# Kernel optimization log

Hardware: AMD Instinct MI355X
Metric: run time of the kernel (lower is better)

Reference implementation:

```python
import jax, jax.numpy as jnp
import numpy as np
from jax import lax

B, L, D = 2, 1024, 1024
INTER = 2816  # _find_multiple(round(4.0*1024*2/3), 256)
K, PAD = 3, 1
S = 32  # sqrt(L)
K2 = K * K


def setup_inputs() -> dict:
    key = jax.random.key(0)
    ks = jax.random.split(key, 7)
    x = jax.random.normal(ks[0], (B, L, D), dtype=jnp.float32)
    w_gate_up = jax.random.normal(ks[1], (2 * INTER, D), dtype=jnp.float32) / np.sqrt(D)
    w_metric = jax.random.normal(ks[2], (7, INTER, 3, 3), dtype=jnp.float32) / np.sqrt(INTER * 9)
    b_metric = jax.random.normal(ks[3], (7,), dtype=jnp.float32) * 0.01
    conv_w = jax.random.normal(ks[4], (INTER, 1, K, K), dtype=jnp.float32) / K
    conv_b = jnp.zeros((INTER,), dtype=jnp.float32)
    w_down = jax.random.normal(ks[5], (D, INTER), dtype=jnp.float32) / np.sqrt(INTER)
    return {"x": x, "w_gate_up": w_gate_up, "w_metric": w_metric,
            "b_metric": b_metric, "conv_w": conv_w, "conv_b": conv_b,
            "w_down": w_down}


def _metric_offsets(x2d, w_metric, b_metric):
    # Finsler-Randers style metric: 2x2 linear map M, drift vector, tanh scale.
    p = lax.conv_general_dilated(x2d, w_metric, (1, 1), 'SAME',
                                 dimension_numbers=('NCHW', 'OIHW', 'NCHW'))
    p = p + b_metric[None, :, None, None]  # [B,7,S,S]
    m00, m01, m10, m11 = p[:, 0], p[:, 1], p[:, 2], p[:, 3]
    dr_y, dr_x = p[:, 4], p[:, 5]
    scale = jnp.tanh(p[:, 6])
    ky = (jnp.arange(K) - PAD).astype(x2d.dtype)
    py = jnp.repeat(ky, K)   # (K2,) kernel-tap dy
    px = jnp.tile(ky, K)     # (K2,) kernel-tap dx
    pyb = py[None, :, None, None]
    pxb = px[None, :, None, None]
    off_y = scale[:, None] * (m00[:, None] * pyb + m01[:, None] * pxb) + dr_y[:, None]
    off_x = scale[:, None] * (m10[:, None] * pyb + m11[:, None] * pxb) + dr_x[:, None]
    return off_y, off_x, py, px  # offsets: [B,K2,S,S]


def _deform_depthwise(x2d, off_y, off_x, py, px, conv_w, conv_b):
    # Sampling positions per output pixel & kernel tap: [B,K2,S,S]
    iy = jnp.arange(S, dtype=x2d.dtype)
    pos_y = iy[None, None, :, None] + py[None, :, None, None] + off_y
    pos_x = iy[None, None, None, :] + px[None, :, None, None] + off_x
    y0 = jnp.floor(pos_y)
    x0 = jnp.floor(pos_x)
    ty = pos_y - y0
    tx = pos_x - x0
    y0i = y0.astype(jnp.int32)
    x0i = x0.astype(jnp.int32)
    flat = x2d.reshape(B, INTER, S * S)

    def corner(yy, xx):
        valid = ((yy >= 0) & (yy < S) & (xx >= 0) & (xx < S)).astype(x2d.dtype)
        idx = (jnp.clip(yy, 0, S - 1) * S + jnp.clip(xx, 0, S - 1)).reshape(B, 1, -1)
        v = jnp.take_along_axis(flat, idx, axis=2).reshape(B, INTER, K2, S, S)
        return v * valid[:, None]

    w00 = ((1 - ty) * (1 - tx))[:, None]
    w01 = ((1 - ty) * tx)[:, None]
    w10 = (ty * (1 - tx))[:, None]
    w11 = (ty * tx)[:, None]
    acc = w00 * corner(y0i, x0i)
    acc = acc + w01 * corner(y0i, x0i + 1)
    acc = acc + w10 * corner(y0i + 1, x0i)
    acc = acc + w11 * corner(y0i + 1, x0i + 1)
    out = jnp.einsum('bckij,ck->bcij', acc, conv_w.reshape(INTER, K2))
    return out + conv_b[None, :, None, None]


def reference(x, w_gate_up, w_metric, b_metric, conv_w, conv_b, w_down):
    gu = jnp.einsum('bld,fd->blf', x, w_gate_up)          # [B,L,2*inter]
    gate, up = jnp.split(gu, 2, axis=-1)
    x_ffn = jax.nn.silu(gate) * up                         # [B,L,inter]
    x2d = x_ffn.transpose(0, 2, 1).reshape(B, INTER, S, S)
    off_y, off_x, py, px = _metric_offsets(x2d, w_metric, b_metric)
    out2d = _deform_depthwise(x2d, off_y, off_x, py, px, conv_w, conv_b)
    grid_out = out2d.reshape(B, INTER, L).transpose(0, 2, 1)
    return jnp.einsum('blf,df->bld', grid_out, w_down)
```

## Files before the change

### kernel.cpp

```cpp
#include <hip/hip_runtime.h>
#include <hip/hip_bf16.h>
#include <cstdint>
#include <cstddef>
#include <type_traits>

#define INTER 2816

typedef __bf16 bf16x8 __attribute__((ext_vector_type(8)));
typedef float f32x4 __attribute__((ext_vector_type(4)));
typedef unsigned short u16x8 __attribute__((ext_vector_type(8)));
using bf16 = __hip_bfloat16;
using u16 = unsigned short;

__device__ __forceinline__ u16 f2bu(float f) {
  bf16 h = __float2bfloat16(f);
  return *reinterpret_cast<u16*>(&h);
}
__device__ __forceinline__ float bu2f(u16 u) {
  bf16 h = *reinterpret_cast<bf16*>(&u);
  return __bfloat162float(h);
}

__device__ __forceinline__ void async16(const u16* g, u16* l) {
  __builtin_amdgcn_global_load_lds(
      (const __attribute__((address_space(1))) unsigned int*)g,
      (__attribute__((address_space(3))) unsigned int*)l, 16, 0, 0);
}

__device__ __forceinline__ void stage8(u16* dst, const float* src) {
  const float4 a = *(const float4*)(src);
  const float4 b = *(const float4*)(src + 4);
  u16 tmp[8] = {f2bu(a.x), f2bu(a.y), f2bu(a.z), f2bu(a.w),
                f2bu(b.x), f2bu(b.y), f2bu(b.z), f2bu(b.w)};
  *(uint4*)dst = *(uint4*)tmp;
}

__global__ __launch_bounds__(256)
void prep_all(const float* __restrict__ x, const float* __restrict__ wgu,
              const float* __restrict__ wd, const float* __restrict__ w_metric,
              const float* __restrict__ conv_w, u16* __restrict__ xbf,
              u16* __restrict__ wgubf, u16* __restrict__ wdbf,
              u16* __restrict__ wm2, float* __restrict__ cwT) {
  constexpr size_t S0 = (size_t)2048 * 1024;
  constexpr size_t S1 = (size_t)5632 * 1024;
  constexpr size_t S2 = (size_t)1024 * 2816;
  constexpr size_t NCONV_THREADS = (S0 + S1 + S2) / 8;
  const size_t t = (size_t)blockIdx.x * 256 + threadIdx.x;
  if (t < NCONV_THREADS) {
    const size_t e0 = t * 8;
    const float* src;
    u16* dst;
    size_t off;
    if (e0 < S0) {
      src = x; dst = xbf; off = e0;
    } else if (e0 < S0 + S1) {
      src = wgu; dst = wgubf; off = e0 - S0;
    } else {
      src = wd; dst = wdbf; off = e0 - S0 - S1;
    }
    stage8(dst + off, src + off);
  } else {
    const unsigned p = (unsigned)(t - NCONV_THREADS);
    const unsigned y = p / 2816u;
    const unsigned c = p - y * 2816u;
    if (y < 128) {
      float v = 0.f;
      if (y < 63) {
        const unsigned o = y / 9, tap = y - o * 9;
        v = w_metric[((size_t)o * INTER + c) * 9 + tap];
      }
      wm2[(size_t)y * INTER + c] = f2bu(v);
    } else {
      const unsigned k = y - 128;
      cwT[(size_t)k * INTER + c] = conv_w[(size_t)c * 9 + k];
    }
  }
}

template <typename OT>
__global__ __launch_bounds__(256, 3)
void gemm_nt(const u16* __restrict__ A, int lda, const u16* __restrict__ Bt,
             int ldb, OT* __restrict__ C, int M, int ldc, int K) {
  __shared__ u16 As[128 * 32];
  __shared__ u16 Bs[128 * 32];
  const size_t koff = (size_t)blockIdx.z * K;
  A += koff;
  Bt += koff;
  C += (size_t)blockIdx.z * M * ldc;
  const int m0 = blockIdx.x * 128;
  const int n0 = blockIdx.y * 128;
  const int tid = threadIdx.x;
  const int lane = tid & 63;
  const int wv = tid >> 6;
  const int wm = wv & 1, wn = wv >> 1;
  const int lr = lane & 15;
  const int lq = lane >> 4;

  f32x4 acc[4][4];
#pragma unroll
  for (int i = 0; i < 4; ++i)
#pragma unroll
    for (int j = 0; j < 4; ++j) acc[i][j] = (f32x4){0.f, 0.f, 0.f, 0.f};

  const int srow = tid >> 2;
  const int scol = (tid & 3) * 8;
  const u16* gA0 = A + (size_t)(m0 + srow) * lda + scol;
  const u16* gA1 = A + (size_t)(m0 + 64 + srow) * lda + scol;
  const u16* gB0 = Bt + (size_t)(n0 + srow) * ldb + scol;
  const u16* gB1 = Bt + (size_t)(n0 + 64 + srow) * ldb + scol;
  u16* lA0 = As + tid * 8;
  u16* lA1 = As + 2048 + tid * 8;
  u16* lB0 = Bs + tid * 8;
  u16* lB1 = Bs + 2048 + tid * 8;

  for (int kb = 0; kb < K; kb += 32) {
    async16(gA0 + kb, lA0);
    async16(gA1 + kb, lA1);
    async16(gB0 + kb, lB0);
    async16(gB1 + kb, lB1);
    __syncthreads();
    bf16x8 af[4], bfr[4];
#pragma unroll
    for (int i = 0; i < 4; ++i)
      af[i] = *(const bf16x8*)(&As[(wm * 64 + i * 16 + lr) * 32 + lq * 8]);
#pragma unroll
    for (int j = 0; j < 4; ++j)
      bfr[j] = *(const bf16x8*)(&Bs[(wn * 64 + j * 16 + lr) * 32 + lq * 8]);
#pragma unroll
    for (int i = 0; i < 4; ++i)
#pragma unroll
      for (int j = 0; j < 4; ++j)
        acc[i][j] = __builtin_amdgcn_mfma_f32_16x16x32_bf16(af[i], bfr[j],
                                                            acc[i][j], 0, 0, 0);
    __syncthreads();
  }

#pragma unroll
  for (int i = 0; i < 4; ++i)
#pragma unroll
    for (int j = 0; j < 4; ++j) {
      const int col = n0 + wn * 64 + j * 16 + lr;
#pragma unroll
      for (int r = 0; r < 4; ++r) {
        const int row = m0 + wm * 64 + i * 16 + lq * 4 + r;
        const float v = acc[i][j][r];
        if constexpr (std::is_same_v<OT, float>) {
          C[(size_t)row * ldc + col] = v;
        } else {
          C[(size_t)row * ldc + col] = f2bu(v);
        }
      }
    }
}

__global__ void reduce4(const float* __restrict__ q2, float* __restrict__ out) {
  const size_t i = ((size_t)blockIdx.x * 256 + threadIdx.x) * 4;
  const size_t S = (size_t)2048 * 1024;
  float4 a = *(const float4*)(q2 + i);
  const float4 b = *(const float4*)(q2 + S + i);
  const float4 c = *(const float4*)(q2 + 2 * S + i);
  const float4 d = *(const float4*)(q2 + 3 * S + i);
  a.x += b.x + c.x + d.x;
  a.y += b.y + c.y + d.y;
  a.z += b.z + c.z + d.z;
  a.w += b.w + c.w + d.w;
  *(float4*)(out + i) = a;
}

__global__ __launch_bounds__(256, 3)
void gateup_gemm(const u16* __restrict__ x, const u16* __restrict__ wgu,
                 u16* __restrict__ xffn) {
  constexpr int K = 1024;
  __shared__ u16 As[128 * 32];
  __shared__ u16 Bgs[64 * 32];
  __shared__ u16 Bus[64 * 32];
  const int m0 = blockIdx.x * 128;
  const int n0 = blockIdx.y * 64;
  const int tid = threadIdx.x;
  const int lane = tid & 63;
  const int wv = tid >> 6;
  const int wm = wv & 1, wn = wv >> 1;
  const int lr = lane & 15;
  const int lq = lane >> 4;

  f32x4 accg[4][2], accu[4][2];
#pragma unroll
  for (int i = 0; i < 4; ++i)
#pragma unroll
    for (int j = 0; j < 2; ++j) {
      accg[i][j] = (f32x4){0.f, 0.f, 0.f, 0.f};
      accu[i][j] = (f32x4){0.f, 0.f, 0.f, 0.f};
    }

  const int srow = tid >> 2;
  const int scol = (tid & 3) * 8;
  const u16* gA0 = x + (size_t)(m0 + srow) * K + scol;
  const u16* gA1 = x + (size_t)(m0 + 64 + srow) * K + scol;
  const u16* gBg = wgu + (size_t)(n0 + srow) * K + scol;
  const u16* gBu = wgu + (size_t)(INTER + n0 + srow) * K + scol;
  u16* lA0 = As + tid * 8;
  u16* lA1 = As + 2048 + tid * 8;
  u16* lBg = Bgs + tid * 8;
  u16* lBu = Bus + tid * 8;

  for (int kb = 0; kb < K; kb += 32) {
    async16(gA0 + kb, lA0);
    async16(gA1 + kb, lA1);
    async16(gBg + kb, lBg);
    async16(gBu + kb, lBu);
    __syncthreads();
    bf16x8 af[4], bg[2], bu[2];
#pragma unroll
    for (int i = 0; i < 4; ++i)
      af[i] = *(const bf16x8*)(&As[(wm * 64 + i * 16 + lr) * 32 + lq * 8]);
#pragma unroll
    for (int j = 0; j < 2; ++j) {
      bg[j] = *(const bf16x8*)(&Bgs[(wn * 32 + j * 16 + lr) * 32 + lq * 8]);
      bu[j] = *(const bf16x8*)(&Bus[(wn * 32 + j * 16 + lr) * 32 + lq * 8]);
    }
#pragma unroll
    for (int i = 0; i < 4; ++i)
#pragma unroll
      for (int j = 0; j < 2; ++j) {
        accg[i][j] = __builtin_amdgcn_mfma_f32_16x16x32_bf16(af[i], bg[j],
                                                             accg[i][j], 0, 0, 0);
        accu[i][j] = __builtin_amdgcn_mfma_f32_16x16x32_bf16(af[i], bu[j],
                                                             accu[i][j], 0, 0, 0);
      }
    __syncthreads();
  }

#pragma unroll
  for (int i = 0; i < 4; ++i)
#pragma unroll
    for (int j = 0; j < 2; ++j) {
      const int col = n0 + wn * 32 + j * 16 + lr;
#pragma unroll
      for (int r = 0; r < 4; ++r) {
        const int row = m0 + wm * 64 + i * 16 + lq * 4 + r;
        const float g = accg[i][j][r];
        const float u = accu[i][j][r];
        const float s = g / (1.f + __expf(-g));
        xffn[(size_t)row * INTER + col] = f2bu(s * u);
      }
    }
}

__global__ __launch_bounds__(64)
void offsets_fused(const float* __restrict__ q,
                   const float* __restrict__ b_metric,
                   int4* __restrict__ samp) {
  __shared__ float lds[130 * 65];
  const int chunk = blockIdx.x;
  const int b = chunk >> 4;
  const int c0 = (chunk & 15) * 64;
  const int t = threadIdx.x;

  for (int v = t; v < 130 * 16; v += 64) {
    const int row = v >> 4;
    const int c4 = (v & 15) * 4;
    int pg = c0 - 33 + row;
    pg = min(max(pg, 0), 1023);
    const float* src = q + ((size_t)b * 1024 + pg) * 128 + c4;
    float4 s = *(const float4*)(src);
#pragma unroll
    for (int ks = 1; ks < 8; ++ks) {
      const float4 vv = *(const float4*)(src + (size_t)ks * 2048 * 128);
      s.x += vv.x; s.y += vv.y; s.z += vv.z; s.w += vv.w;
    }
    float* d = &lds[row * 65 + c4];
    d[0] = s.x; d[1] = s.y; d[2] = s.z; d[3] = s.w;
  }
  __syncthreads();

  const int pix = c0 + t;
  const int i = pix >> 5, j = pix & 31;
  float p[7];
#pragma unroll
  for (int o = 0; o < 7; ++o) p[o] = b_metric[o];
#pragma unroll
  for (int tap = 0; tap < 9; ++tap) {
    const int dy = tap / 3 - 1, dx = tap % 3 - 1;
    const int ii = i + dy, jj = j + dx;
    if ((unsigned)ii < 32u && (unsigned)jj < 32u) {
      const float* r = &lds[(t + 33 + dy * 32 + dx) * 65 + tap];
#pragma unroll
      for (int o = 0; o < 7; ++o) p[o] += r[o * 9];
    }
  }
  const float m00 = p[0], m01 = p[1], m10 = p[2], m11 = p[3];
  const float dry = p[4], drx = p[5];
  const float sc = tanhf(p[6]);
#pragma unroll
  for (int k = 0; k < 9; ++k) {
    const float pyk = (float)(k / 3 - 1), pxk = (float)(k % 3 - 1);
    const float offy = sc * (m00 * pyk + m01 * pxk) + dry;
    const float offx = sc * (m10 * pyk + m11 * pxk) + drx;
    const float posy = (float)i + pyk + offy;
    const float posx = (float)j + pxk + offx;
    const float y0f = floorf(posy), x0f = floorf(posx);
    int4 s;
    s.x = (int)y0f;
    s.y = (int)x0f;
    s.z = __float_as_int(posy - y0f);
    s.w = __float_as_int(posx - x0f);
    samp[((size_t)b * 9 + k) * 1024 + pix] = s;
  }
}

__global__ __launch_bounds__(256)
void deform_kernel(const u16* __restrict__ xffn,
                   const int4* __restrict__ samp,
                   const float* __restrict__ cwT,
                   const float* __restrict__ conv_b,
                   u16* __restrict__ gridout) {
  const unsigned t = blockIdx.x * 256 + threadIdx.x;
  const unsigned pix = t / 352u;
  const unsigned cv = t - pix * 352u;
  const int c0 = cv * 8;
  const int b = pix >> 10, l = pix & 1023;

  float acc[8];
  {
    const float4 b0 = *(const float4*)(&conv_b[c0]);
    const float4 b1 = *(const float4*)(&conv_b[c0 + 4]);
    acc[0] = b0.x; acc[1] = b0.y; acc[2] = b0.z; acc[3] = b0.w;
    acc[4] = b1.x; acc[5] = b1.y; acc[6] = b1.z; acc[7] = b1.w;
  }
  const size_t pixbase = (size_t)b * 1024;
#pragma unroll
  for (int k = 0; k < 9; ++k) {
    const int4 s = samp[((size_t)b * 9 + k) * 1024 + l];
    const int y0 = s.x, x0 = s.y;
    const float ty = __int_as_float(s.z), tx = __int_as_float(s.w);
    const int y1 = y0 + 1, x1 = x0 + 1;
    const float vy0 = ((unsigned)y0 < 32u) ? 1.f : 0.f;
    const float vy1 = ((unsigned)y1 < 32u) ? 1.f : 0.f;
    const float vx0 = ((unsigned)x0 < 32u) ? 1.f : 0.f;
    const float vx1 = ((unsigned)x1 < 32u) ? 1.f : 0.f;
    const float w00 = (1.f - ty) * (1.f - tx) * vy0 * vx0;
    const float w01 = (1.f - ty) * tx * vy0 * vx1;
    const float w10 = ty * (1.f - tx) * vy1 * vx0;
    const float w11 = ty * tx * vy1 * vx1;
    const int cy0 = min(max(y0, 0), 31), cy1 = min(max(y1, 0), 31);
    const int cx0 = min(max(x0, 0), 31), cx1 = min(max(x1, 0), 31);
    const u16x8 v00 = *(const u16x8*)(&xffn[(pixbase + cy0 * 32 + cx0) * INTER + c0]);
    const u16x8 v01 = *(const u16x8*)(&xffn[(pixbase + cy0 * 32 + cx1) * INTER + c0]);
    const u16x8 v10 = *(const u16x8*)(&xffn[(pixbase + cy1 * 32 + cx0) * INTER + c0]);
    const u16x8 v11 = *(const u16x8*)(&xffn[(pixbase + cy1 * 32 + cx1) * INTER + c0]);
    const float4 cwa = *(const float4*)(&cwT[(size_t)k * INTER + c0]);
    const float4 cwb = *(const float4*)(&cwT[(size_t)k * INTER + c0 + 4]);
    const float cw[8] = {cwa.x, cwa.y, cwa.z, cwa.w, cwb.x, cwb.y, cwb.z, cwb.w};
#pragma unroll
    for (int e = 0; e < 8; ++e) {
      const float bl = w00 * bu2f(v00[e]) + w01 * bu2f(v01[e]) +
                       w10 * bu2f(v10[e]) + w11 * bu2f(v11[e]);
      acc[e] += bl * cw[e];
    }
  }
  u16 outv[8];
#pragma unroll
  for (int e = 0; e < 8; ++e) outv[e] = f2bu(acc[e]);
  *(uint4*)(&gridout[(pixbase + l) * INTER + c0]) = *(uint4*)outv;
}

extern "C" void kernel_launch(void* const* d_in, const int* in_sizes, int n_in,
                              void* d_out, int out_size, void* d_ws,
                              size_t ws_size, hipStream_t stream) {
  const float* x         = (const float*)d_in[0];
  const float* w_gate_up = (const float*)d_in[1];
  const float* w_metric  = (const float*)d_in[2];
  const float* b_metric  = (const float*)d_in[3];
  const float* conv_w    = (const float*)d_in[4];
  const float* conv_b    = (const float*)d_in[5];
  const float* w_down    = (const float*)d_in[6];
  float* out = (float*)d_out;

  char* w = (char*)d_ws;
  u16* gridout  = (u16*)(w);
  float* q2     = (float*)(w + (12u << 20));
  u16* xffn     = (u16*)(w + (12u << 20));
  u16* xbf      = (u16*)(w + (24u << 20));
  u16* wgubf    = (u16*)(w + (28u << 20) + (256u << 10));
  float* q_conv = (float*)(w + (28u << 20) + (256u << 10));
  u16* wm2      = (u16*)(w + (40u << 20));
  float* cwT    = (float*)(w + (41u << 20));
  int4* samp    = (int4*)(w + (42u << 20));
  u16* wdbf     = (u16*)(w + (44u << 20));

  prep_all<<<6755, 256, 0, stream>>>(x, w_gate_up, w_down, w_metric, conv_w,
                                     xbf, wgubf, wdbf, wm2, cwT);
  gateup_gemm<<<dim3(16, 44), 256, 0, stream>>>(xbf, wgubf, xffn);
  gemm_nt<float><<<dim3(16, 1, 8), 256, 0, stream>>>(
      xffn, INTER, wm2, INTER, q_conv, 2048, 128, 352);
  offsets_fused<<<32, 64, 0, stream>>>(q_conv, b_metric, samp);
  deform_kernel<<<2816, 256, 0, stream>>>(xffn, samp, cwT, conv_b, gridout);
  gemm_nt<float><<<dim3(16, 8, 4), 256, 0, stream>>>(
      gridout, INTER, wdbf, INTER, q2, 2048, 1024, 704);
  reduce4<<<2048, 256, 0, stream>>>(q2, out);
}
```

Before: 211.1 us.

## Replace split-K partial buffer and reduce kernel with atomics; widen gate-up tile

The down-projection split-K GEMM now adds its partial results straight into the zeroed output with float atomics. This drops the 4-slice fp32 partial buffer and the separate reduce4 kernel, at the cost of a memset and atomic traffic. The gate/up GEMM tile also grows from 64 to 128 columns, doubling the accumulators per wave and lowering occupancy to 2 blocks. The larger tile is meant to raise arithmetic intensity per loaded A tile.

Result: slower. 234.6 us (+11.1%).

```diff
diff --git a/kernel.cpp b/kernel.cpp
--- a/kernel.cpp
+++ b/kernel.cpp
@@ -77,7 +77,7 @@
   }
 }
 
-template <typename OT>
+template <typename OT, bool ATOMIC>
 __global__ __launch_bounds__(256, 3)
 void gemm_nt(const u16* __restrict__ A, int lda, const u16* __restrict__ Bt,
              int ldb, OT* __restrict__ C, int M, int ldc, int K) {
@@ -86,7 +86,7 @@
   const size_t koff = (size_t)blockIdx.z * K;
   A += koff;
   Bt += koff;
-  C += (size_t)blockIdx.z * M * ldc;
+  if constexpr (!ATOMIC) C += (size_t)blockIdx.z * M * ldc;
   const int m0 = blockIdx.x * 128;
   const int n0 = blockIdx.y * 128;
   const int tid = threadIdx.x;
@@ -144,7 +144,9 @@
       for (int r = 0; r < 4; ++r) {
         const int row = m0 + wm * 64 + i * 16 + lq * 4 + r;
         const float v = acc[i][j][r];
-        if constexpr (std::is_same_v<OT, float>) {
+        if constexpr (ATOMIC) {
+          unsafeAtomicAdd((float*)&C[(size_t)row * ldc + col], v);
+        } else if constexpr (std::is_same_v<OT, float>) {
           C[(size_t)row * ldc + col] = v;
         } else {
           C[(size_t)row * ldc + col] = f2bu(v);
@@ -153,29 +155,15 @@
     }
 }
 
-__global__ void reduce4(const float* __restrict__ q2, float* __restrict__ out) {
-  const size_t i = ((size_t)blockIdx.x * 256 + threadIdx.x) * 4;
-  const size_t S = (size_t)2048 * 1024;
-  float4 a = *(const float4*)(q2 + i);
-  const float4 b = *(const float4*)(q2 + S + i);
-  const float4 c = *(const float4*)(q2 + 2 * S + i);
-  const float4 d = *(const float4*)(q2 + 3 * S + i);
-  a.x += b.x + c.x + d.x;
-  a.y += b.y + c.y + d.y;
-  a.z += b.z + c.z + d.z;
-  a.w += b.w + c.w + d.w;
-  *(float4*)(out + i) = a;
-}
-
-__global__ __launch_bounds__(256, 3)
+__global__ __launch_bounds__(256, 2)
 void gateup_gemm(const u16* __restrict__ x, const u16* __restrict__ wgu,
                  u16* __restrict__ xffn) {
   constexpr int K = 1024;
   __shared__ u16 As[128 * 32];
-  __shared__ u16 Bgs[64 * 32];
-  __shared__ u16 Bus[64 * 32];
+  __shared__ u16 Bgs[128 * 32];
+  __shared__ u16 Bus[128 * 32];
   const int m0 = blockIdx.x * 128;
-  const int n0 = blockIdx.y * 64;
+  const int n0 = blockIdx.y * 128;
   const int tid = threadIdx.x;
   const int lane = tid & 63;
   const int wv = tid >> 6;
@@ -183,11 +171,11 @@
   const int lr = lane & 15;
   const int lq = lane >> 4;
 
-  f32x4 accg[4][2], accu[4][2];
+  f32x4 accg[4][4], accu[4][4];
 #pragma unroll
   for (int i = 0; i < 4; ++i)
 #pragma unroll
-    for (int j = 0; j < 2; ++j) {
+    for (int j = 0; j < 4; ++j) {
       accg[i][j] = (f32x4){0.f, 0.f, 0.f, 0.f};
       accu[i][j] = (f32x4){0.f, 0.f, 0.f, 0.f};
     }
@@ -196,32 +184,38 @@
   const int scol = (tid & 3) * 8;
   const u16* gA0 = x + (size_t)(m0 + srow) * K + scol;
   const u16* gA1 = x + (size_t)(m0 + 64 + srow) * K + scol;
-  const u16* gBg = wgu + (size_t)(n0 + srow) * K + scol;
-  const u16* gBu = wgu + (size_t)(INTER + n0 + srow) * K + scol;
+  const u16* gBg0 = wgu + (size_t)(n0 + srow) * K + scol;
+  const u16* gBg1 = wgu + (size_t)(n0 + 64 + srow) * K + scol;
+  const u16* gBu0 = wgu + (size_t)(INTER + n0 + srow) * K + scol;
+  const u16* gBu1 = wgu + (size_t)(INTER + n0 + 64 + srow) * K + scol;
   u16* lA0 = As + tid * 8;
   u16* lA1 = As + 2048 + tid * 8;
-  u16* lBg = Bgs + tid * 8;
-  u16* lBu = Bus + tid * 8;
+  u16* lBg0 = Bgs + tid * 8;
+  u16* lBg1 = Bgs + 2048 + tid * 8;
+  u16* lBu0 = Bus + tid * 8;
+  u16* lBu1 = Bus + 2048 + tid * 8;
 
   for (int kb = 0; kb < K; kb += 32) {
     async16(gA0 + kb, lA0);
     async16(gA1 + kb, lA1);
-    async16(gBg + kb, lBg);
-    async16(gBu + kb, lBu);
+    async16(gBg0 + kb, lBg0);
+    async16(gBg1 + kb, lBg1);
+    async16(gBu0 + kb, lBu0);
+    async16(gBu1 + kb, lBu1);
     __syncthreads();
-    bf16x8 af[4], bg[2], bu[2];
+    bf16x8 af[4], bg[4], bu[4];
 #pragma unroll
     for (int i = 0; i < 4; ++i)
       af[i] = *(const bf16x8*)(&As[(wm * 64 + i * 16 + lr) * 32 + lq * 8]);
 #pragma unroll
-    for (int j = 0; j < 2; ++j) {
-      bg[j] = *(const bf16x8*)(&Bgs[(wn * 32 + j * 16 + lr) * 32 + lq * 8]);
-      bu[j] = *(const bf16x8*)(&Bus[(wn * 32 + j * 16 + lr) * 32 + lq * 8]);
+    for (int j = 0; j < 4; ++j) {
+      bg[j] = *(const bf16x8*)(&Bgs[(wn * 64 + j * 16 + lr) * 32 + lq * 8]);
+      bu[j] = *(const bf16x8*)(&Bus[(wn * 64 + j * 16 + lr) * 32 + lq * 8]);
     }
 #pragma unroll
     for (int i = 0; i < 4; ++i)
 #pragma unroll
-      for (int j = 0; j < 2; ++j) {
+      for (int j = 0; j < 4; ++j) {
         accg[i][j] = __builtin_amdgcn_mfma_f32_16x16x32_bf16(af[i], bg[j],
                                                              accg[i][j], 0, 0, 0);
         accu[i][j] = __builtin_amdgcn_mfma_f32_16x16x32_bf16(af[i], bu[j],
@@ -233,8 +227,8 @@
 #pragma unroll
   for (int i = 0; i < 4; ++i)
 #pragma unroll
-    for (int j = 0; j < 2; ++j) {
-      const int col = n0 + wn * 32 + j * 16 + lr;
+    for (int j = 0; j < 4; ++j) {
+      const int col = n0 + wn * 64 + j * 16 + lr;
 #pragma unroll
       for (int r = 0; r < 4; ++r) {
         const int row = m0 + wm * 64 + i * 16 + lq * 4 + r;
@@ -378,7 +372,6 @@
 
   char* w = (char*)d_ws;
   u16* gridout  = (u16*)(w);
-  float* q2     = (float*)(w + (12u << 20));
   u16* xffn     = (u16*)(w + (12u << 20));
   u16* xbf      = (u16*)(w + (24u << 20));
   u16* wgubf    = (u16*)(w + (28u << 20) + (256u << 10));
@@ -388,14 +381,14 @@
   int4* samp    = (int4*)(w + (42u << 20));
   u16* wdbf     = (u16*)(w + (44u << 20));
 
+  hipMemsetAsync(out, 0, (size_t)2048 * 1024 * sizeof(float), stream);
   prep_all<<<6755, 256, 0, stream>>>(x, w_gate_up, w_down, w_metric, conv_w,
                                      xbf, wgubf, wdbf, wm2, cwT);
-  gateup_gemm<<<dim3(16, 44), 256, 0, stream>>>(xbf, wgubf, xffn);
-  gemm_nt<float><<<dim3(16, 1, 8), 256, 0, stream>>>(
+  gateup_gemm<<<dim3(16, 22), 256, 0, stream>>>(xbf, wgubf, xffn);
+  gemm_nt<float, false><<<dim3(16, 1, 8), 256, 0, stream>>>(
       xffn, INTER, wm2, INTER, q_conv, 2048, 128, 352);
   offsets_fused<<<32, 64, 0, stream>>>(q_conv, b_metric, samp);
   deform_kernel<<<2816, 256, 0, stream>>>(xffn, samp, cwT, conv_b, gridout);
-  gemm_nt<float><<<dim3(16, 8, 4), 256, 0, stream>>>(
-      gridout, INTER, wdbf, INTER, q2, 2048, 1024, 704);
-  reduce4<<<2048, 256, 0, stream>>>(q2, out);
-}
+  gemm_nt<float, true><<<dim3(16, 8, 4), 256, 0, stream>>>(
+      gridout, INTER, wdbf, INTER, out, 2048, 1024, 704);
+}
```

## Double-buffer LDS tiles in both GEMM kernels to overlap loads with MFMA

Applied to the files above, without the earlier changes.

Both bf16 GEMM kernels now keep two LDS buffers per operand. The next K-slice is loaded asynchronously while MFMAs run on the current slice, and the trailing barrier per iteration is dropped. This aims to hide global-to-LDS latency behind compute. It doubles shared memory per block, and gateup's occupancy hint drops from 3 to 2. A single barrier per iteration may be unsafe if async loads into the next buffer race with slow waves still reading it, though the alternating buffers make that less likely.

Result: no change. 212.0 us (+0.4%).

```diff
diff --git a/kernel.cpp b/kernel.cpp
--- a/kernel.cpp
+++ b/kernel.cpp
@@ -81,8 +81,8 @@
 __global__ __launch_bounds__(256, 3)
 void gemm_nt(const u16* __restrict__ A, int lda, const u16* __restrict__ Bt,
              int ldb, OT* __restrict__ C, int M, int ldc, int K) {
-  __shared__ u16 As[128 * 32];
-  __shared__ u16 Bs[128 * 32];
+  __shared__ u16 As[2][128 * 32];
+  __shared__ u16 Bs[2][128 * 32];
   const size_t koff = (size_t)blockIdx.z * K;
   A += koff;
   Bt += koff;
@@ -108,31 +108,39 @@
   const u16* gA1 = A + (size_t)(m0 + 64 + srow) * lda + scol;
   const u16* gB0 = Bt + (size_t)(n0 + srow) * ldb + scol;
   const u16* gB1 = Bt + (size_t)(n0 + 64 + srow) * ldb + scol;
-  u16* lA0 = As + tid * 8;
-  u16* lA1 = As + 2048 + tid * 8;
-  u16* lB0 = Bs + tid * 8;
-  u16* lB1 = Bs + 2048 + tid * 8;
-
-  for (int kb = 0; kb < K; kb += 32) {
-    async16(gA0 + kb, lA0);
-    async16(gA1 + kb, lA1);
-    async16(gB0 + kb, lB0);
-    async16(gB1 + kb, lB1);
+
+  const int nIter = K >> 5;
+  async16(gA0, &As[0][tid * 8]);
+  async16(gA1, &As[0][2048 + tid * 8]);
+  async16(gB0, &Bs[0][tid * 8]);
+  async16(gB1, &Bs[0][2048 + tid * 8]);
+
+  for (int it = 0; it < nIter; ++it) {
     __syncthreads();
+    const int cur = it & 1;
+    const u16* as = As[cur];
+    const u16* bs = Bs[cur];
+    if (it + 1 < nIter) {
+      const int kb = (it + 1) << 5;
+      const int nxt = cur ^ 1;
+      async16(gA0 + kb, &As[nxt][tid * 8]);
+      async16(gA1 + kb, &As[nxt][2048 + tid * 8]);
+      async16(gB0 + kb, &Bs[nxt][tid * 8]);
+      async16(gB1 + kb, &Bs[nxt][2048 + tid * 8]);
+    }
     bf16x8 af[4], bfr[4];
 #pragma unroll
     for (int i = 0; i < 4; ++i)
-      af[i] = *(const bf16x8*)(&As[(wm * 64 + i * 16 + lr) * 32 + lq * 8]);
+      af[i] = *(const bf16x8*)(&as[(wm * 64 + i * 16 + lr) * 32 + lq * 8]);
 #pragma unroll
     for (int j = 0; j < 4; ++j)
-      bfr[j] = *(const bf16x8*)(&Bs[(wn * 64 + j * 16 + lr) * 32 + lq * 8]);
+      bfr[j] = *(const bf16x8*)(&bs[(wn * 64 + j * 16 + lr) * 32 + lq * 8]);
 #pragma unroll
     for (int i = 0; i < 4; ++i)
 #pragma unroll
       for (int j = 0; j < 4; ++j)
         acc[i][j] = __builtin_amdgcn_mfma_f32_16x16x32_bf16(af[i], bfr[j],
                                                             acc[i][j], 0, 0, 0);
-    __syncthreads();
   }
 
 #pragma unroll
@@ -167,13 +175,13 @@
   *(float4*)(out + i) = a;
 }
 
-__global__ __launch_bounds__(256, 3)
+__global__ __launch_bounds__(256, 2)
 void gateup_gemm(const u16* __restrict__ x, const u16* __restrict__ wgu,
                  u16* __restrict__ xffn) {
   constexpr int K = 1024;
-  __shared__ u16 As[128 * 32];
-  __shared__ u16 Bgs[64 * 32];
-  __shared__ u16 Bus[64 * 32];
+  __shared__ u16 As[2][128 * 32];
+  __shared__ u16 Bgs[2][64 * 32];
+  __shared__ u16 Bus[2][64 * 32];
   const int m0 = blockIdx.x * 128;
   const int n0 = blockIdx.y * 64;
   const int tid = threadIdx.x;
@@ -198,25 +206,35 @@
   const u16* gA1 = x + (size_t)(m0 + 64 + srow) * K + scol;
   const u16* gBg = wgu + (size_t)(n0 + srow) * K + scol;
   const u16* gBu = wgu + (size_t)(INTER + n0 + srow) * K + scol;
-  u16* lA0 = As + tid * 8;
-  u16* lA1 = As + 2048 + tid * 8;
-  u16* lBg = Bgs + tid * 8;
-  u16* lBu = Bus + tid * 8;
-
-  for (int kb = 0; kb < K; kb += 32) {
-    async16(gA0 + kb, lA0);
-    async16(gA1 + kb, lA1);
-    async16(gBg + kb, lBg);
-    async16(gBu + kb, lBu);
+
+  constexpr int nIter = K >> 5;
+  async16(gA0, &As[0][tid * 8]);
+  async16(gA1, &As[0][2048 + tid * 8]);
+  async16(gBg, &Bgs[0][tid * 8]);
+  async16(gBu, &Bus[0][tid * 8]);
+
+  for (int it = 0; it < nIter; ++it) {
     __syncthreads();
+    const int cur = it & 1;
+    const u16* as = As[cur];
+    const u16* bgs = Bgs[cur];
+    const u16* bus = Bus[cur];
+    if (it + 1 < nIter) {
+      const int kb = (it + 1) << 5;
+      const int nxt = cur ^ 1;
+      async16(gA0 + kb, &As[nxt][tid * 8]);
+      async16(gA1 + kb, &As[nxt][2048 + tid * 8]);
+      async16(gBg + kb, &Bgs[nxt][tid * 8]);
+      async16(gBu + kb, &Bus[nxt][tid * 8]);
+    }
     bf16x8 af[4], bg[2], bu[2];
 #pragma unroll
     for (int i = 0; i < 4; ++i)
-      af[i] = *(const bf16x8*)(&As[(wm * 64 + i * 16 + lr) * 32 + lq * 8]);
+      af[i] = *(const bf16x8*)(&as[(wm * 64 + i * 16 + lr) * 32 + lq * 8]);
 #pragma unroll
     for (int j = 0; j < 2; ++j) {
-      bg[j] = *(const bf16x8*)(&Bgs[(wn * 32 + j * 16 + lr) * 32 + lq * 8]);
-      bu[j] = *(const bf16x8*)(&Bus[(wn * 32 + j * 16 + lr) * 32 + lq * 8]);
+      bg[j] = *(const bf16x8*)(&bgs[(wn * 32 + j * 16 + lr) * 32 + lq * 8]);
+      bu[j] = *(const bf16x8*)(&bus[(wn * 32 + j * 16 + lr) * 32 + lq * 8]);
     }
 #pragma unroll
     for (int i = 0; i < 4; ++i)
@@ -227,7 +245,6 @@
         accu[i][j] = __builtin_amdgcn_mfma_f32_16x16x32_bf16(af[i], bu[j],
                                                              accu[i][j], 0, 0, 0);
       }
-    __syncthreads();
   }
 
 #pragma unroll
```
